# Performance work log

Hardware: AMD Instinct MI355X
Metric: run time of the kernel (lower is better)

The kernel has to match this reference:

```python
import jax, jax.numpy as jnp
import numpy as np

B, S, D, F, E = 4, 1024, 768, 3072, 8


def setup_inputs() -> dict:
    key = jax.random.key(0)
    k0, k1, k2, k3 = jax.random.split(key, 4)
    hidden_states = jax.random.normal(k0, (B, S, D), dtype=jnp.float32)
    w_router = jax.random.normal(k1, (D, E), dtype=jnp.float32) * 0.02
    w1 = jax.random.normal(k2, (E, D, F), dtype=jnp.float32) * 0.02
    b1 = jnp.zeros((E, F), dtype=jnp.float32)
    w2 = jax.random.normal(k3, (E, F, D), dtype=jnp.float32) * 0.02
    b2 = jnp.zeros((E, D), dtype=jnp.float32)
    return {"hidden_states": hidden_states, "w_router": w_router,
            "w1": w1, "b1": b1, "w2": w2, "b2": b2}


def reference(hidden_states, w_router, w1, b1, w2, b2):
    # Switch-style top-1 router: logits -> softmax -> one-hot mask + max prob
    router_logits = jnp.einsum("bsd,de->bse", hidden_states, w_router)
    router_probs_full = jax.nn.softmax(router_logits, axis=-1)
    expert_index = jnp.argmax(router_probs_full, axis=-1)            # [B,S] int
    router_probs = jnp.max(router_probs_full, axis=-1, keepdims=True)  # [B,S,1]
    router_mask = jax.nn.one_hot(expert_index, E, dtype=hidden_states.dtype)  # [B,S,E]

    # Dispatch/compute/combine: each token goes to exactly one expert FFN.
    # Loop over the small fixed expert set (E=8), combine via the one-hot mask;
    # math is identical to the gather -> expert FFN -> scatter of the original.
    out = jnp.zeros_like(hidden_states)
    for e in range(E):
        h = jax.nn.relu(jnp.einsum("bsd,df->bsf", hidden_states, w1[e]) + b1[e])
        h = jnp.einsum("bsf,fd->bsd", h, w2[e]) + b2[e]
        out = out + router_mask[..., e:e + 1] * h

    hidden_out = router_probs * out  # scale by top-1 router prob, as in original
    return hidden_out, router_logits, expert_index
```

## Files before the change

kernel.cpp:

```cpp
#include <hip/hip_runtime.h>
#include <hip/hip_bf16.h>

#define T_TOK 4096
#define DIM   768
#define FF    3072
#define NE    8
#define MAXTILES 48

typedef __attribute__((ext_vector_type(8))) short bf16x8;
typedef __attribute__((ext_vector_type(4))) short bf16x4;
typedef __attribute__((ext_vector_type(4))) float f32x4;
typedef __attribute__((ext_vector_type(2))) float f32x2;

typedef __attribute__((address_space(1))) void gvoid_t;
typedef __attribute__((address_space(3))) void lvoid_t;

__device__ __forceinline__ void g2l16(const void* g, void* l) {
    __builtin_amdgcn_global_load_lds((gvoid_t*)(void*)g, (lvoid_t*)l, 16, 0, 0);
}

#define WAIT_VM0() __builtin_amdgcn_s_waitcnt(0x0F70)
#define WAIT_VM2() __builtin_amdgcn_s_waitcnt(0x0F72)
#define WAIT_VM3() __builtin_amdgcn_s_waitcnt(0x0F73)
#define RAW_BARRIER() asm volatile("s_barrier" ::: "memory")

__device__ __forceinline__ unsigned short f2bf(float f) {
    union { float f; unsigned int u; } v; v.f = f;
    unsigned int u = v.u;
    u += 0x7FFFu + ((u >> 16) & 1u);
    return (unsigned short)(u >> 16);
}

__device__ __forceinline__ bf16x8 pack8(f32x4 a, f32x4 b) {
    bf16x8 r;
    r[0] = (short)f2bf(a[0]); r[1] = (short)f2bf(a[1]);
    r[2] = (short)f2bf(a[2]); r[3] = (short)f2bf(a[3]);
    r[4] = (short)f2bf(b[0]); r[5] = (short)f2bf(b[1]);
    r[6] = (short)f2bf(b[2]); r[7] = (short)f2bf(b[3]);
    return r;
}

__global__ __launch_bounds__(256) void k_router(
    const float* __restrict__ x, const float* __restrict__ wr,
    float* __restrict__ out_logits, float* __restrict__ out_eidx,
    float* __restrict__ probs, int* __restrict__ eidx_i,
    int* __restrict__ counts, int* __restrict__ bucket,
    unsigned short* __restrict__ Xb, float* __restrict__ outh)
{
    int tok  = (blockIdx.x * 256 + threadIdx.x) >> 6;
    int lane = threadIdx.x & 63;
    if (tok >= T_TOK) return;
    {
        float* o = outh + (size_t)tok * DIM;
        #pragma unroll
        for (int j = 0; j < DIM / 256; j++)
            *(f32x4*)(o + j * 256 + lane * 4) = (f32x4)0.f;
    }
    const float* xr = x + (size_t)tok * DIM;
    unsigned short* xbr = Xb + (size_t)tok * DIM;
    float acc[NE];
    #pragma unroll
    for (int e = 0; e < NE; e++) acc[e] = 0.f;
    #pragma unroll
    for (int j = 0; j < DIM / 64; j++) {
        int d = j * 64 + lane;
        float xv = xr[d];
        xbr[d] = f2bf(xv);
        const float* wrow = wr + (size_t)d * NE;
        #pragma unroll
        for (int e = 0; e < NE; e++) acc[e] += xv * wrow[e];
    }
    #pragma unroll
    for (int e = 0; e < NE; e++) {
        #pragma unroll
        for (int off = 32; off >= 1; off >>= 1)
            acc[e] += __shfl_xor(acc[e], off);
    }
    if (lane == 0) {
        float mx = acc[0]; int mi = 0;
        #pragma unroll
        for (int e = 1; e < NE; e++) if (acc[e] > mx) { mx = acc[e]; mi = e; }
        float se = 0.f;
        #pragma unroll
        for (int e = 0; e < NE; e++) se += __expf(acc[e] - mx);
        #pragma unroll
        for (int e = 0; e < NE; e++) out_logits[(size_t)tok * NE + e] = acc[e];
        out_eidx[tok] = (float)mi;
        eidx_i[tok] = mi;
        probs[tok] = 1.f / se;
        int pos = atomicAdd(&counts[mi], 1);
        bucket[mi * T_TOK + pos] = tok;
    }
}

__global__ void k_compact(const int* __restrict__ counts, int* __restrict__ offsets,
                          int* __restrict__ bucket, int* __restrict__ sorted)
{
    __shared__ int soff[NE + 1];
    if (threadIdx.x == 0) {
        int s = 0;
        for (int e = 0; e < NE; e++) { soff[e] = s; s += counts[e]; }
        soff[NE] = s;
        for (int e = 0; e <= NE; e++) offsets[e] = soff[e];
    }
    __syncthreads();
    for (int e = 0; e < NE; e++) {
        int c = counts[e], o = soff[e];
        for (int i = threadIdx.x; i < c; i += blockDim.x)
            sorted[o + i] = bucket[e * T_TOK + i];
    }
    __syncthreads();
    if (threadIdx.x == 0) {
        int nt = 0;
        for (int e = 0; e < NE; e++) {
            int c = counts[e];
            for (int t = 0; t * 128 < c && nt < MAXTILES; t++)
                bucket[nt++] = (e << 8) | t;
        }
        for (int i = nt; i < MAXTILES; i++) bucket[i] = -1;
    }
}

__global__ __launch_bounds__(256) void k_tconv(
    const float* __restrict__ w1, unsigned short* __restrict__ wt1,
    const float* __restrict__ w2, unsigned short* __restrict__ wt2)
{
    int R, C, c0, r0;
    const float* in;
    unsigned short* out;
    if (blockIdx.z < NE) {
        R = DIM; C = FF;
        in  = w1  + (size_t)blockIdx.z * R * C;
        out = wt1 + (size_t)blockIdx.z * R * C;
        c0 = blockIdx.x * 64; r0 = blockIdx.y * 64;
    } else {
        R = FF; C = DIM;
        in  = w2  + (size_t)(blockIdx.z - NE) * R * C;
        out = wt2 + (size_t)(blockIdx.z - NE) * R * C;
        c0 = blockIdx.y * 64; r0 = blockIdx.x * 64;
    }
    __shared__ unsigned short t[64][72];
    const int tr = threadIdx.x >> 2, tc = (threadIdx.x & 3) * 16;
    const float* src = in + (size_t)(r0 + tr) * C + c0 + tc;
    f32x4 v0 = *(const f32x4*)(src);
    f32x4 v1 = *(const f32x4*)(src + 4);
    f32x4 v2 = *(const f32x4*)(src + 8);
    f32x4 v3 = *(const f32x4*)(src + 12);
    const int xb = (tc >> 4) & 3;
    const int pr = (((tr >> 3) ^ xb) & 7) * 8 + (tr & 7);
    #pragma unroll
    for (int j = 0; j < 4; j++) {
        t[tc + j][pr]      = f2bf(v0[j]);
        t[tc + 4 + j][pr]  = f2bf(v1[j]);
        t[tc + 8 + j][pr]  = f2bf(v2[j]);
        t[tc + 12 + j][pr] = f2bf(v3[j]);
    }
    __syncthreads();
    const int oc = threadIdx.x >> 2, orr = (threadIdx.x & 3) * 16;
    const int rx = (oc >> 4) & 3;
    const int p0 = ((((orr >> 3) + 0) ^ rx) & 7) * 8;
    const int p1 = ((((orr >> 3) + 1) ^ rx) & 7) * 8;
    bf16x8 o0 = *(const bf16x8*)&t[oc][p0];
    bf16x8 o1 = *(const bf16x8*)&t[oc][p1];
    unsigned short* dst = out + (size_t)(c0 + oc) * R + r0 + orr;
    *(bf16x8*)(dst)     = o0;
    *(bf16x8*)(dst + 8) = o1;
}

__global__ __launch_bounds__(512, 4) void k_gemm1(
    const unsigned short* __restrict__ Xb, const unsigned short* __restrict__ wt1,
    const float* __restrict__ b1, const int* __restrict__ sorted,
    const int* __restrict__ counts, const int* __restrict__ offsets,
    const int* __restrict__ tile_tab, unsigned short* __restrict__ Hbuf)
{
    const int tv = tile_tab[blockIdx.y];
    if (tv < 0) return;
    const int e  = tv >> 8;
    const int ti = tv & 255;
    const int cnt = counts[e];
    const int n0 = blockIdx.x * 256;
    const int off = offsets[e];
    const int rbase = ti * 128;
    const int tid = threadIdx.x, lane = tid & 63, wave = tid >> 6;
    const int wm = wave >> 2, wn = wave & 3;

    __shared__ unsigned short As[3][128][32];
    __shared__ unsigned short Bs[3][256][32];

    const int lr = lane >> 2;
    const int ls = (lane & 3) * 8;

    const unsigned short* wB = wt1 + (size_t)e * FF * DIM;
    const unsigned short* gp[3];
    unsigned short* lb[3];
    int lstep[3];
    #pragma unroll
    for (int j = 0; j < 3; j++) {
        int c = wave * 3 + j;
        if (c < 8) {
            int rr = rbase + c * 16 + lr; if (rr >= cnt) rr = rbase;
            gp[j] = Xb + (size_t)sorted[off + rr] * DIM + ls;
            lb[j] = &As[0][c * 16][0];
            lstep[j] = 128 * 32;
        } else {
            gp[j] = wB + (size_t)(n0 + (c - 8) * 16 + lr) * DIM + ls;
            lb[j] = &Bs[0][(c - 8) * 16][0];
            lstep[j] = 256 * 32;
        }
    }

    f32x4 acc[4][4];
    #pragma unroll
    for (int i = 0; i < 4; i++)
        #pragma unroll
        for (int j = 0; j < 4; j++) acc[i][j] = (f32x4)0.f;

    const int lrow = lane & 15, kq = lane >> 4;
    const int NIT = DIM / 32;

#define STAGE1(bufi, ko) do { \
    g2l16(gp[0] + (ko), lb[0] + (bufi) * lstep[0]); \
    g2l16(gp[1] + (ko), lb[1] + (bufi) * lstep[1]); \
    g2l16(gp[2] + (ko), lb[2] + (bufi) * lstep[2]); \
} while (0)

    STAGE1(0, 0);
    __syncthreads();
    STAGE1(1, 32);

    for (int it = 0; it < NIT; ++it) {
        const int buf = it % 3;
        if (it > 0) {
            if (it + 1 < NIT) WAIT_VM3(); else WAIT_VM0();
            RAW_BARRIER();
        }
        if (it + 2 < NIT) {
            STAGE1((it + 2) % 3, (it + 2) * 32);
        }
        bf16x8 af[4], bfv[4];
        #pragma unroll
        for (int i = 0; i < 4; i++)
            af[i] = *(const bf16x8*)&As[buf][wm * 64 + i * 16 + lrow][kq * 8];
        #pragma unroll
        for (int j = 0; j < 4; j++)
            bfv[j] = *(const bf16x8*)&Bs[buf][wn * 64 + j * 16 + lrow][kq * 8];
        #pragma unroll
        for (int mi = 0; mi < 4; mi++)
            #pragma unroll
            for (int ni = 0; ni < 4; ni++)
                acc[mi][ni] = __builtin_amdgcn_mfma_f32_16x16x32_bf16(
                    af[mi], bfv[ni], acc[mi][ni], 0, 0, 0);
    }
#undef STAGE1

    const int quad = lane >> 4;
    #pragma unroll
    for (int ni = 0; ni < 4; ni++) {
        int gn = n0 + wn * 64 + ni * 16 + lrow;
        float bias = b1[e * FF + gn];
        #pragma unroll
        for (int mi = 0; mi < 4; mi++) {
            f32x4 v = acc[mi][ni];
            #pragma unroll
            for (int r = 0; r < 4; r++) {
                int ml = rbase + wm * 64 + mi * 16 + quad * 4 + r;
                if (ml < cnt) {
                    float h = v[r] + bias; h = h > 0.f ? h : 0.f;
                    Hbuf[(size_t)(off + ml) * FF + gn] = f2bf(h);
                }
            }
        }
    }
}

__global__ __launch_bounds__(512, 6) void k_gemm2(
    const unsigned short* __restrict__ Hbuf, const unsigned short* __restrict__ wt2,
    const float* __restrict__ b2, const int* __restrict__ sorted,
    const int* __restrict__ counts, const int* __restrict__ offsets,
    const int* __restrict__ tile_tab, const float* __restrict__ probs,
    float* __restrict__ outh)
{
    const int lid = blockIdx.x + 6 * blockIdx.y + 288 * blockIdx.z;
    const int xcd = lid & 7;
    const int j_  = lid >> 3;
    const int m   = j_ % 6;
    const int gg  = (j_ / 6) * 8 + xcd;
    const int by  = gg % MAXTILES;
    const int kc  = gg / MAXTILES;

    const int tv = tile_tab[by];
    if (tv < 0) return;
    const int e  = tv >> 8;
    const int ti = tv & 255;
    const int cnt = counts[e];
    const int n0 = m * 128;
    const int off = offsets[e];
    const int rbase = ti * 128;
    const int tid = threadIdx.x, lane = tid & 63, wave = tid >> 6;
    const int wm = wave >> 1, wn = wave & 1;

    __shared__ unsigned short As[3][128][32];
    __shared__ unsigned short Bs[3][128][32];
    __shared__ int   s_tok[128];
    __shared__ float s_prob[128];

    if (tid < 128) {
        int rr = rbase + tid; if (rr >= cnt) rr = rbase;
        int tk = sorted[off + rr];
        s_tok[tid]  = tk;
        s_prob[tid] = probs[tk];
    }

    const int lr = lane >> 2, ls = (lane & 3) * 8;

    const unsigned short* wB = wt2 + (size_t)e * DIM * FF;
    const unsigned short* gp[2];
    unsigned short* lb[2];
    #pragma unroll
    for (int j = 0; j < 2; j++) {
        int c = wave * 2 + j;
        if (c < 8) {
            int rr = rbase + c * 16 + lr; if (rr >= cnt) rr = rbase;
            gp[j] = Hbuf + (size_t)(off + rr) * FF + kc * 1024 + ls;
            lb[j] = &As[0][c * 16][0];
        } else {
            gp[j] = wB + (size_t)(n0 + (c - 8) * 16 + lr) * FF + kc * 1024 + ls;
            lb[j] = &Bs[0][(c - 8) * 16][0];
        }
    }
    const int lstep = 128 * 32;

    f32x4 acc[2][4];
    #pragma unroll
    for (int i = 0; i < 2; i++)
        #pragma unroll
        for (int j = 0; j < 4; j++) acc[i][j] = (f32x4)0.f;

    const int lrow = lane & 15, kq = lane >> 4;
    const int NIT = 1024 / 32;

#define STAGE2(bufi, ko) do { \
    g2l16(gp[0] + (ko), lb[0] + (bufi) * lstep); \
    g2l16(gp[1] + (ko), lb[1] + (bufi) * lstep); \
} while (0)

    STAGE2(0, 0);
    __syncthreads();
    STAGE2(1, 32);

    for (int it = 0; it < NIT; ++it) {
        const int buf = it % 3;
        if (it > 0) {
            if (it + 1 < NIT) WAIT_VM2(); else WAIT_VM0();
            RAW_BARRIER();
        }
        if (it + 2 < NIT) {
            STAGE2((it + 2) % 3, (it + 2) * 32);
        }
        bf16x8 af[2], bfv[4];
        #pragma unroll
        for (int i = 0; i < 2; i++)
            af[i] = *(const bf16x8*)&As[buf][wm * 32 + i * 16 + lrow][kq * 8];
        #pragma unroll
        for (int j = 0; j < 4; j++)
            bfv[j] = *(const bf16x8*)&Bs[buf][wn * 64 + j * 16 + lrow][kq * 8];
        #pragma unroll
        for (int mi = 0; mi < 2; mi++)
            #pragma unroll
            for (int ni = 0; ni < 4; ni++)
                acc[mi][ni] = __builtin_amdgcn_mfma_f32_16x16x32_bf16(
                    af[mi], bfv[ni], acc[mi][ni], 0, 0, 0);
    }
#undef STAGE2

    const int quad = lane >> 4;
    #pragma unroll
    for (int ni = 0; ni < 4; ni++) {
        int gn = n0 + wn * 64 + ni * 16 + lrow;
        float bias = (kc == 0) ? b2[e * DIM + gn] : 0.f;
        #pragma unroll
        for (int mi = 0; mi < 2; mi++) {
            f32x4 v = acc[mi][ni];
            #pragma unroll
            for (int r = 0; r < 4; r++) {
                int mloc = wm * 32 + mi * 16 + quad * 4 + r;
                if (rbase + mloc < cnt) {
                    atomicAdd(&outh[(size_t)s_tok[mloc] * DIM + gn],
                              (v[r] + bias) * s_prob[mloc]);
                }
            }
        }
    }
}

__global__ __launch_bounds__(256) void k_gather_fb(
    const float* __restrict__ x, const int* __restrict__ sorted,
    unsigned short* __restrict__ Xg)
{
    int g0 = (blockIdx.x * 256 + threadIdx.x) * 8;
    if (g0 >= T_TOK * DIM) return;
    int row = g0 / DIM, col = g0 - row * DIM;
    const float* src = x + (size_t)sorted[row] * DIM + col;
    f32x4 a = *(const f32x4*)(src);
    f32x4 b = *(const f32x4*)(src + 4);
    *(bf16x8*)(Xg + (size_t)row * DIM + col) = pack8(a, b);
}

__global__ __launch_bounds__(256, 3) void k_gemm1_fb(
    const unsigned short* __restrict__ Xg, const float* __restrict__ w1,
    const float* __restrict__ b1, const int* __restrict__ counts,
    const int* __restrict__ offsets, unsigned short* __restrict__ Hbuf)
{
    const int e   = blockIdx.y >> 5;
    const int ti  = blockIdx.y & 31;
    const int cnt = counts[e];
    if (ti * 128 >= cnt) return;
    const int n0    = blockIdx.x * 128;
    const int off   = offsets[e];
    const int rbase = ti * 128;
    const int rmax  = cnt - rbase - 1;
    const int tid   = threadIdx.x;
    const int lane  = tid & 63;
    const int wave  = tid >> 6;
    const int wm = wave >> 1, wn = wave & 1;
    __shared__ unsigned short As[128][72];
    __shared__ unsigned short Bs[128][72];
    const float* w1e = w1 + (size_t)e * DIM * FF;
    f32x4 acc[4][4];
    #pragma unroll
    for (int i = 0; i < 4; i++)
        #pragma unroll
        for (int j = 0; j < 4; j++) acc[i][j] = (f32x4)0.f;
    const int arow = tid >> 1, aseg = tid & 1;
    const int are  = (arow <= rmax) ? arow : 0;
    const unsigned short* abase = Xg + (size_t)(off + rbase + are) * DIM + aseg * 32;
    const int kb = tid >> 5, nb = tid & 31;
    const float* bbase = w1e + (size_t)kb * 8 * FF + n0 + nb * 4;
    bf16x8 aR[4];
    f32x4  bR[8];
    #pragma unroll
    for (int j = 0; j < 4; j++) aR[j] = *(const bf16x8*)(abase + j * 8);
    #pragma unroll
    for (int r = 0; r < 8; r++) bR[r] = *(const f32x4*)(bbase + (size_t)r * FF);
    const int lrow = lane & 15, kq = lane >> 4;
    for (int it = 0; it < DIM / 64; ++it) {
        __syncthreads();
        #pragma unroll
        for (int j = 0; j < 4; j++)
            *(bf16x8*)&As[arow][aseg * 32 + j * 8] = aR[j];
        #pragma unroll
        for (int j = 0; j < 4; j++) {
            bf16x8 c;
            #pragma unroll
            for (int r = 0; r < 8; r++) c[r] = (short)f2bf(bR[r][j]);
            *(bf16x8*)&Bs[nb * 4 + j][kb * 8] = c;
        }
        __syncthreads();
        if (it + 1 < DIM / 64) {
            const unsigned short* an = abase + (it + 1) * 64;
            #pragma unroll
            for (int j = 0; j < 4; j++) aR[j] = *(const bf16x8*)(an + j * 8);
            const float* bn = bbase + (size_t)(it + 1) * 64 * FF;
            #pragma unroll
            for (int r = 0; r < 8; r++) bR[r] = *(const f32x4*)(bn + (size_t)r * FF);
        }
        #pragma unroll
        for (int ks = 0; ks < 2; ks++) {
            bf16x8 af[4], bfr[4];
            #pragma unroll
            for (int i = 0; i < 4; i++)
                af[i] = *(const bf16x8*)&As[wm * 64 + i * 16 + lrow][ks * 32 + kq * 8];
            #pragma unroll
            for (int i = 0; i < 4; i++)
                bfr[i] = *(const bf16x8*)&Bs[wn * 64 + i * 16 + lrow][ks * 32 + kq * 8];
            #pragma unroll
            for (int mi = 0; mi < 4; mi++)
                #pragma unroll
                for (int ni = 0; ni < 4; ni++)
                    acc[mi][ni] = __builtin_amdgcn_mfma_f32_16x16x32_bf16(
                        af[mi], bfr[ni], acc[mi][ni], 0, 0, 0);
        }
    }
    const int quad = lane >> 4;
    #pragma unroll
    for (int ni = 0; ni < 4; ni++) {
        int gn = n0 + wn * 64 + ni * 16 + lrow;
        float bias = b1[e * FF + gn];
        #pragma unroll
        for (int mi = 0; mi < 4; mi++) {
            f32x4 v = acc[mi][ni];
            #pragma unroll
            for (int r = 0; r < 4; r++) {
                int ml = wm * 64 + mi * 16 + quad * 4 + r;
                if (rbase + ml < cnt) {
                    float h = v[r] + bias;
                    h = h > 0.f ? h : 0.f;
                    Hbuf[(size_t)(off + rbase + ml) * FF + gn] = f2bf(h);
                }
            }
        }
    }
}

__global__ __launch_bounds__(256, 4) void k_gemm2_fb(
    const unsigned short* __restrict__ Hbuf, const float* __restrict__ w2,
    const float* __restrict__ b2, const int* __restrict__ sorted,
    const int* __restrict__ counts, const int* __restrict__ offsets,
    const float* __restrict__ probs, float* __restrict__ outh)
{
    const int e   = blockIdx.y >> 5;
    const int ti  = blockIdx.y & 31;
    const int cnt = counts[e];
    if (ti * 128 >= cnt) return;
    const int n0    = blockIdx.x * 64;
    const int off   = offsets[e];
    const int rbase = ti * 128;
    const int rmax  = cnt - rbase - 1;
    const int tid   = threadIdx.x;
    const int lane  = tid & 63;
    const int wave  = tid >> 6;
    const int wm = wave >> 1, wn = wave & 1;
    __shared__ unsigned short As[128][72];
    __shared__ unsigned short Bs[64][72];
    __shared__ int   s_tok[128];
    __shared__ float s_prob[128];
    if (tid < 128) {
        int r = rbase + tid;
        int tk = sorted[off + ((r < cnt) ? r : rbase)];
        s_tok[tid]  = tk;
        s_prob[tid] = probs[tk];
    }
    const float* w2e = w2 + (size_t)e * FF * DIM;
    f32x4 acc[4][2];
    #pragma unroll
    for (int i = 0; i < 4; i++)
        #pragma unroll
        for (int j = 0; j < 2; j++) acc[i][j] = (f32x4)0.f;
    const int arow = tid >> 1, aseg = tid & 1;
    const int are  = (arow <= rmax) ? arow : 0;
    const unsigned short* abase = Hbuf + (size_t)(off + rbase + are) * FF + aseg * 32;
    const int kb = tid >> 5, nb = tid & 31;
    const float* bbase = w2e + (size_t)kb * 8 * DIM + n0 + nb * 2;
    bf16x8 aR[4];
    f32x2  bR[8];
    #pragma unroll
    for (int j = 0; j < 4; j++) aR[j] = *(const bf16x8*)(abase + j * 8);
    #pragma unroll
    for (int r = 0; r < 8; r++) bR[r] = *(const f32x2*)(bbase + (size_t)r * DIM);
    const int lrow = lane & 15, kq = lane >> 4;
    for (int it = 0; it < FF / 64; ++it) {
        __syncthreads();
        #pragma unroll
        for (int j = 0; j < 4; j++)
            *(bf16x8*)&As[arow][aseg * 32 + j * 8] = aR[j];
        {
            bf16x8 c0, c1;
            #pragma unroll
            for (int r = 0; r < 8; r++) { c0[r] = (short)f2bf(bR[r][0]); c1[r] = (short)f2bf(bR[r][1]); }
            *(bf16x8*)&Bs[nb * 2 + 0][kb * 8] = c0;
            *(bf16x8*)&Bs[nb * 2 + 1][kb * 8] = c1;
        }
        __syncthreads();
        if (it + 1 < FF / 64) {
            const unsigned short* an = abase + (it + 1) * 64;
            #pragma unroll
            for (int j = 0; j < 4; j++) aR[j] = *(const bf16x8*)(an + j * 8);
            const float* bn = bbase + (size_t)(it + 1) * 64 * DIM;
            #pragma unroll
            for (int r = 0; r < 8; r++) bR[r] = *(const f32x2*)(bn + (size_t)r * DIM);
        }
        #pragma unroll
        for (int ks = 0; ks < 2; ks++) {
            bf16x8 af[4], bfr[2];
            #pragma unroll
            for (int i = 0; i < 4; i++)
                af[i] = *(const bf16x8*)&As[wm * 64 + i * 16 + lrow][ks * 32 + kq * 8];
            #pragma unroll
            for (int i = 0; i < 2; i++)
                bfr[i] = *(const bf16x8*)&Bs[wn * 32 + i * 16 + lrow][ks * 32 + kq * 8];
            #pragma unroll
            for (int mi = 0; mi < 4; mi++)
                #pragma unroll
                for (int ni = 0; ni < 2; ni++)
                    acc[mi][ni] = __builtin_amdgcn_mfma_f32_16x16x32_bf16(
                        af[mi], bfr[ni], acc[mi][ni], 0, 0, 0);
        }
    }
    const int quad = lane >> 4;
    #pragma unroll
    for (int ni = 0; ni < 2; ni++) {
        int gn = n0 + wn * 32 + ni * 16 + lrow;
        float bias = b2[e * DIM + gn];
        #pragma unroll
        for (int mi = 0; mi < 4; mi++) {
            f32x4 v = acc[mi][ni];
            #pragma unroll
            for (int r = 0; r < 4; r++) {
                int ml = wm * 64 + mi * 16 + quad * 4 + r;
                if (rbase + ml < cnt) {
                    outh[(size_t)s_tok[ml] * DIM + gn] = (v[r] + bias) * s_prob[ml];
                }
            }
        }
    }
}

extern "C" void kernel_launch(void* const* d_in, const int* in_sizes, int n_in,
                              void* d_out, int out_size, void* d_ws, size_t ws_size,
                              hipStream_t stream) {
    (void)in_sizes; (void)n_in; (void)out_size;
    const float* x  = (const float*)d_in[0];
    const float* wr = (const float*)d_in[1];
    const float* w1 = (const float*)d_in[2];
    const float* b1 = (const float*)d_in[3];
    const float* w2 = (const float*)d_in[4];
    const float* b2 = (const float*)d_in[5];

    float* out_hidden = (float*)d_out;
    float* out_logits = out_hidden + (size_t)T_TOK * DIM;
    float* out_eidx   = out_logits + (size_t)T_TOK * NE;

    char* ws = (char*)d_ws;
    int*   counts  = (int*)(ws + 0);
    int*   offsets = (int*)(ws + 64);
    float* probs   = (float*)(ws + 128);
    int*   eidx_i  = (int*)(ws + 16512);
    int*   sorted  = (int*)(ws + 32896);
    int*   bucket  = (int*)(ws + 49280);
    int*   tile_tab = bucket;
    unsigned short* Xb   = (unsigned short*)(ws + 180352);
    unsigned short* Hbuf = (unsigned short*)(ws + 6471808);
    unsigned short* wt1  = (unsigned short*)(ws + 31637632);
    unsigned short* wt2  = (unsigned short*)(ws + 69386368);
    const size_t NEED = 107135104;

    hipMemsetAsync(counts, 0, 32, stream);

    if (ws_size >= NEED) {
        k_router<<<dim3(T_TOK / 4), dim3(256), 0, stream>>>(
            x, wr, out_logits, out_eidx, probs, eidx_i, counts, bucket, Xb, out_hidden);
        k_compact<<<dim3(1), dim3(256), 0, stream>>>(counts, offsets, bucket, sorted);
        k_tconv<<<dim3(48, 12, 2 * NE), dim3(256), 0, stream>>>(w1, wt1, w2, wt2);
        k_gemm1<<<dim3(FF / 256, MAXTILES), dim3(512), 0, stream>>>(
            Xb, wt1, b1, sorted, counts, offsets, tile_tab, Hbuf);
        k_gemm2<<<dim3(DIM / 128, MAXTILES, 3), dim3(512), 0, stream>>>(
            Hbuf, wt2, b2, sorted, counts, offsets, tile_tab, probs, out_hidden);
    } else {
        k_router<<<dim3(T_TOK / 4), dim3(256), 0, stream>>>(
            x, wr, out_logits, out_eidx, probs, eidx_i, counts, bucket, Xb, out_hidden);
        k_compact<<<dim3(1), dim3(256), 0, stream>>>(counts, offsets, bucket, sorted);
        k_gather_fb<<<dim3(T_TOK * DIM / 8 / 256), dim3(256), 0, stream>>>(x, sorted, Xb);
        k_gemm1_fb<<<dim3(FF / 128, NE * 32), dim3(256), 0, stream>>>(
            Xb, w1, b1, counts, offsets, Hbuf);
        k_gemm2_fb<<<dim3(DIM / 64, NE * 32), dim3(256), 0, stream>>>(
            Hbuf, w2, b2, sorted, counts, offsets, probs, out_hidden);
    }
}
```

Baseline: 357.5 us.

## Fuse weight transpose-convert into router kernel and drop LDS transpose

```diff
diff --git a/kernel.cpp b/kernel.cpp
--- a/kernel.cpp
+++ b/kernel.cpp
@@ -40,13 +40,58 @@
     return r;
 }
 
-__global__ __launch_bounds__(256) void k_router(
+#define RT_ROUTER_BLKS (T_TOK / 4)
+#define RT_W1_BLKS     1152
+#define RT_W2_BLKS     1152
+__global__ __launch_bounds__(256) void k_rtconv(
     const float* __restrict__ x, const float* __restrict__ wr,
     float* __restrict__ out_logits, float* __restrict__ out_eidx,
     float* __restrict__ probs, int* __restrict__ eidx_i,
     int* __restrict__ counts, int* __restrict__ bucket,
-    unsigned short* __restrict__ Xb, float* __restrict__ outh)
+    unsigned short* __restrict__ Xb, float* __restrict__ outh,
+    const float* __restrict__ w1, unsigned short* __restrict__ wt1,
+    const float* __restrict__ w2, unsigned short* __restrict__ wt2)
 {
+    if (blockIdx.x >= RT_ROUTER_BLKS) {
+        int bid = blockIdx.x - RT_ROUTER_BLKS;
+        const float* in;
+        unsigned short* out;
+        int C, R, n0, r0;
+        if (bid < RT_W1_BLKS) {
+            int e   = bid / 144;
+            int rem = bid - e * 144;
+            n0 = (rem % 12) * 256;
+            r0 = (rem / 12) * 64;
+            C = FF; R = DIM;
+            in  = w1  + (size_t)e * DIM * FF;
+            out = wt1 + (size_t)e * DIM * FF;
+        } else {
+            int t2  = bid - RT_W1_BLKS;
+            int e   = t2 / 144;
+            int rem = t2 - e * 144;
+            n0 = (rem % 3) * 256;
+            r0 = (rem / 3) * 64;
+            C = DIM; R = FF;
+            in  = w2  + (size_t)e * DIM * FF;
+            out = wt2 + (size_t)e * DIM * FF;
+        }
+        const int n = n0 + threadIdx.x;
+        const float* src = in + (size_t)r0 * C + n;
+        unsigned short* dst = out + (size_t)n * R + r0;
+        float v[64];
+        #pragma unroll
+        for (int i = 0; i < 64; i++)
+            v[i] = src[(size_t)i * C];
+        #pragma unroll
+        for (int g = 0; g < 8; g++) {
+            bf16x8 o;
+            #pragma unroll
+            for (int i = 0; i < 8; i++) o[i] = (short)f2bf(v[g * 8 + i]);
+            *(bf16x8*)(dst + g * 8) = o;
+        }
+        return;
+    }
+
     int tok  = (blockIdx.x * 256 + threadIdx.x) >> 6;
     int lane = threadIdx.x & 63;
     if (tok >= T_TOK) return;
@@ -119,52 +164,6 @@
         }
         for (int i = nt; i < MAXTILES; i++) bucket[i] = -1;
     }
-}
-
-__global__ __launch_bounds__(256) void k_tconv(
-    const float* __restrict__ w1, unsigned short* __restrict__ wt1,
-    const float* __restrict__ w2, unsigned short* __restrict__ wt2)
-{
-    int R, C, c0, r0;
-    const float* in;
-    unsigned short* out;
-    if (blockIdx.z < NE) {
-        R = DIM; C = FF;
-        in  = w1  + (size_t)blockIdx.z * R * C;
-        out = wt1 + (size_t)blockIdx.z * R * C;
-        c0 = blockIdx.x * 64; r0 = blockIdx.y * 64;
-    } else {
-        R = FF; C = DIM;
-        in  = w2  + (size_t)(blockIdx.z - NE) * R * C;
-        out = wt2 + (size_t)(blockIdx.z - NE) * R * C;
-        c0 = blockIdx.y * 64; r0 = blockIdx.x * 64;
-    }
-    __shared__ unsigned short t[64][72];
-    const int tr = threadIdx.x >> 2, tc = (threadIdx.x & 3) * 16;
-    const float* src = in + (size_t)(r0 + tr) * C + c0 + tc;
-    f32x4 v0 = *(const f32x4*)(src);
-    f32x4 v1 = *(const f32x4*)(src + 4);
-    f32x4 v2 = *(const f32x4*)(src + 8);
-    f32x4 v3 = *(const f32x4*)(src + 12);
-    const int xb = (tc >> 4) & 3;
-    const int pr = (((tr >> 3) ^ xb) & 7) * 8 + (tr & 7);
-    #pragma unroll
-    for (int j = 0; j < 4; j++) {
-        t[tc + j][pr]      = f2bf(v0[j]);
-        t[tc + 4 + j][pr]  = f2bf(v1[j]);
-        t[tc + 8 + j][pr]  = f2bf(v2[j]);
-        t[tc + 12 + j][pr] = f2bf(v3[j]);
-    }
-    __syncthreads();
-    const int oc = threadIdx.x >> 2, orr = (threadIdx.x & 3) * 16;
-    const int rx = (oc >> 4) & 3;
-    const int p0 = ((((orr >> 3) + 0) ^ rx) & 7) * 8;
-    const int p1 = ((((orr >> 3) + 1) ^ rx) & 7) * 8;
-    bf16x8 o0 = *(const bf16x8*)&t[oc][p0];
-    bf16x8 o1 = *(const bf16x8*)&t[oc][p1];
-    unsigned short* dst = out + (size_t)(c0 + oc) * R + r0 + orr;
-    *(bf16x8*)(dst)     = o0;
-    *(bf16x8*)(dst + 8) = o1;
 }
 
 __global__ __launch_bounds__(512, 4) void k_gemm1(
@@ -637,17 +636,18 @@
     hipMemsetAsync(counts, 0, 32, stream);
 
     if (ws_size >= NEED) {
-        k_router<<<dim3(T_TOK / 4), dim3(256), 0, stream>>>(
-            x, wr, out_logits, out_eidx, probs, eidx_i, counts, bucket, Xb, out_hidden);
+        k_rtconv<<<dim3(RT_ROUTER_BLKS + RT_W1_BLKS + RT_W2_BLKS), dim3(256), 0, stream>>>(
+            x, wr, out_logits, out_eidx, probs, eidx_i, counts, bucket, Xb, out_hidden,
+            w1, wt1, w2, wt2);
         k_compact<<<dim3(1), dim3(256), 0, stream>>>(counts, offsets, bucket, sorted);
-        k_tconv<<<dim3(48, 12, 2 * NE), dim3(256), 0, stream>>>(w1, wt1, w2, wt2);
         k_gemm1<<<dim3(FF / 256, MAXTILES), dim3(512), 0, stream>>>(
             Xb, wt1, b1, sorted, counts, offsets, tile_tab, Hbuf);
         k_gemm2<<<dim3(DIM / 128, MAXTILES, 3), dim3(512), 0, stream>>>(
             Hbuf, wt2, b2, sorted, counts, offsets, tile_tab, probs, out_hidden);
     } else {
-        k_router<<<dim3(T_TOK / 4), dim3(256), 0, stream>>>(
-            x, wr, out_logits, out_eidx, probs, eidx_i, counts, bucket, Xb, out_hidden);
+        k_rtconv<<<dim3(RT_ROUTER_BLKS), dim3(256), 0, stream>>>(
+            x, wr, out_logits, out_eidx, probs, eidx_i, counts, bucket, Xb, out_hidden,
+            w1, (unsigned short*)Xb, w2, (unsigned short*)Xb);
         k_compact<<<dim3(1), dim3(256), 0, stream>>>(counts, offsets, bucket, sorted);
         k_gather_fb<<<dim3(T_TOK * DIM / 8 / 256), dim3(256), 0, stream>>>(x, sorted, Xb);
         k_gemm1_fb<<<dim3(FF / 128, NE * 32), dim3(256), 0, stream>>>(
```

New measurement: 354.8 us. No clear change (-0.8%).
